# Optimization experiments

Hardware: AMD Instinct MI355X
Metric: run time of the kernel (lower is better)

Reference implementation:

```python
import jax, jax.numpy as jnp
import numpy as np

NUM_LEVELS = 6
LEVEL_DIM = 4
LOG2_HASHMAP = 19
HASHMAP_SIZE = 1 << LOG2_HASHMAP
BASE_RES = 16
DESIRED_RES = 512
SPHERE_RADIUS = 500.0
N_RAYS = 1048576
PER_LEVEL_SCALE = float(np.exp(np.log(DESIRED_RES / BASE_RES) / (NUM_LEVELS - 1)))  # = 2.0
PRIMES = (1, 2654435761, 805459861)
# static 8 trilinear corner offsets [8,3]
_CORNERS_NP = np.array([[i, j, k] for i in (0, 1) for j in (0, 1) for k in (0, 1)], dtype=np.int64)


def _level_params(level):
    # torch-ngp / Instant-NGP convention: scale = base * gamma**L - 1, res = ceil(scale)+1
    scale = BASE_RES * (PER_LEVEL_SCALE ** level) - 1.0
    res = int(np.ceil(scale)) + 1
    return scale, res


def hash_grid_encode(coords, table):
    """coords: [N,3] in [0,1]; table: [L, HASHMAP_SIZE, D] -> [N, L*D]."""
    corners_f = jnp.asarray(_CORNERS_NP, dtype=coords.dtype)        # [8,3]
    corners_u = jnp.asarray(_CORNERS_NP, dtype=jnp.uint32)          # [8,3]
    outs = []
    for level in range(NUM_LEVELS):
        scale, res = _level_params(level)
        pos = coords * scale + 0.5                                   # [N,3]
        pos_grid = jnp.floor(pos)
        frac = pos - pos_grid                                        # [N,3] in [0,1)
        pg = pos_grid.astype(jnp.uint32)                             # [N,3]
        cg = pg[:, None, :] + corners_u[None, :, :]                  # [N,8,3]
        if res ** 3 <= HASHMAP_SIZE:
            # dense indexing for coarse levels
            cg = jnp.minimum(cg, jnp.uint32(res - 1))
            idx = cg[..., 0] + cg[..., 1] * jnp.uint32(res) + cg[..., 2] * jnp.uint32(res * res)
        else:
            # spatial hash with xor of primes, table size is a power of two
            h = (cg[..., 0] * jnp.uint32(PRIMES[0])
                 ^ cg[..., 1] * jnp.uint32(PRIMES[1])
                 ^ cg[..., 2] * jnp.uint32(PRIMES[2]))
            idx = h & jnp.uint32(HASHMAP_SIZE - 1)
        feats = table[level][idx.astype(jnp.int32)]                  # [N,8,D] gather
        # trilinear weights: prod over dims of (frac if corner==1 else 1-frac)
        w = jnp.prod(jnp.where(corners_f[None] == 1.0, frac[:, None, :], 1.0 - frac[:, None, :]), axis=-1)  # [N,8]
        outs.append(jnp.sum(feats * w[..., None], axis=1))           # [N,D]
    return jnp.concatenate(outs, axis=-1)                            # [N, L*D]


def setup_inputs() -> dict:
    key = jax.random.key(0)
    k1, k2, k3 = jax.random.split(key, 3)
    view_dirs = jax.random.normal(k1, (N_RAYS, 3), dtype=jnp.float32)
    view_dirs = view_dirs / jnp.linalg.norm(view_dirs, axis=-1, keepdims=True)
    ray_origins = jax.random.normal(k2, (N_RAYS, 3), dtype=jnp.float32)  # cameras near origin, radius >> extent
    table = jax.random.uniform(k3, (NUM_LEVELS, HASHMAP_SIZE, LEVEL_DIM),
                               dtype=jnp.float32, minval=-0.1, maxval=0.1)
    return {"view_dirs": view_dirs, "ray_origins": ray_origins, "table": table}


def reference(view_dirs, ray_origins, table):
    # ray-sphere intersection (a=1 since dirs normalized)
    b = 2.0 * jnp.sum(ray_origins * view_dirs, axis=-1, keepdims=True)
    c = jnp.sum(ray_origins * ray_origins, axis=-1, keepdims=True) - SPHERE_RADIUS ** 2
    disc = b * b - 4.0 * c
    t = (-b + jnp.sqrt(jnp.maximum(disc, 0.0))) / 2.0
    pts = ray_origins + t * view_dirs                                 # [N,3]
    coords = jnp.clip((pts + SPHERE_RADIUS) / (2.0 * SPHERE_RADIUS), 0.0, 1.0)
    return hash_grid_encode(coords, table)                            # [N, 24]
```

## Files before the change

kernel.cpp:

```cpp
#include <hip/hip_runtime.h>

constexpr unsigned kHashmapSize = 1u << 19;
constexpr float kSphereR = 500.0f;

__global__ __launch_bounds__(256)
void sphere_hashgrid_kernel(const float* __restrict__ dirs,
                            const float* __restrict__ orig,
                            const float4* __restrict__ table4,
                            float* __restrict__ out,
                            int n_rays)
{
    int n = blockIdx.x * blockDim.x + threadIdx.x;
    if (n >= n_rays) return;

    float dx = dirs[3 * n + 0], dy = dirs[3 * n + 1], dz = dirs[3 * n + 2];
    float ox = orig[3 * n + 0], oy = orig[3 * n + 1], oz = orig[3 * n + 2];

    float b = 2.0f * ((ox * dx + oy * dy) + oz * dz);
    float c = ((ox * ox + oy * oy) + oz * oz) - kSphereR * kSphereR;
    float disc = b * b - 4.0f * c;
    float t = (-b + sqrtf(fmaxf(disc, 0.0f))) * 0.5f;
    float px = ox + t * dx, py = oy + t * dy, pz = oz + t * dz;

    float cx = fminf(fmaxf((px + kSphereR) / (2.0f * kSphereR), 0.0f), 1.0f);
    float cy = fminf(fmaxf((py + kSphereR) / (2.0f * kSphereR), 0.0f), 1.0f);
    float cz = fminf(fmaxf((pz + kSphereR) / (2.0f * kSphereR), 0.0f), 1.0f);

    constexpr float kScale[6] = {15.f, 31.f, 63.f, 127.f, 255.f, 511.f};
    constexpr unsigned kRes[6] = {16u, 32u, 64u, 128u, 256u, 512u};

    float* outp = out + (size_t)n * 24;

#pragma unroll
    for (int L = 0; L < 6; ++L) {
        const float sc = kScale[L];
        const unsigned res = kRes[L];
        const bool dense = (L < 3);

        float posx = cx * sc + 0.5f;
        float posy = cy * sc + 0.5f;
        float posz = cz * sc + 0.5f;
        float gx_f = floorf(posx), gy_f = floorf(posy), gz_f = floorf(posz);
        float fx = posx - gx_f, fy = posy - gy_f, fz = posz - gz_f;
        unsigned gx = (unsigned)gx_f, gy = (unsigned)gy_f, gz = (unsigned)gz_f;

        const float4* __restrict__ tl = table4 + (size_t)L * kHashmapSize;

        unsigned idx[8];
#pragma unroll
        for (int cr = 0; cr < 8; ++cr) {
            unsigned i = (unsigned)(cr >> 2);
            unsigned j = (unsigned)((cr >> 1) & 1);
            unsigned k = (unsigned)(cr & 1);
            unsigned x = gx + i, y = gy + j, z = gz + k;
            if (dense) {
                x = min(x, res - 1u);
                y = min(y, res - 1u);
                z = min(z, res - 1u);
                idx[cr] = x + y * res + z * res * res;
            } else {
                idx[cr] = (x * 1u ^ y * 2654435761u ^ z * 805459861u) & (kHashmapSize - 1u);
            }
        }

        float4 f[8];
#pragma unroll
        for (int cr = 0; cr < 8; ++cr) f[cr] = tl[idx[cr]];

        float wx[2] = {1.0f - fx, fx};
        float wy[2] = {1.0f - fy, fy};
        float wz[2] = {1.0f - fz, fz};

        float4 acc = make_float4(0.f, 0.f, 0.f, 0.f);
#pragma unroll
        for (int cr = 0; cr < 8; ++cr) {
            float w = (wx[(cr >> 2) & 1] * wy[(cr >> 1) & 1]) * wz[cr & 1];
            acc.x += f[cr].x * w;
            acc.y += f[cr].y * w;
            acc.z += f[cr].z * w;
            acc.w += f[cr].w * w;
        }

        *(float4*)(outp + L * 4) = acc;
    }
}

extern "C" void kernel_launch(void* const* d_in, const int* in_sizes, int n_in,
                              void* d_out, int out_size, void* d_ws, size_t ws_size,
                              hipStream_t stream) {
    const float* dirs = (const float*)d_in[0];
    const float* orig = (const float*)d_in[1];
    const float4* table4 = (const float4*)d_in[2];
    float* out = (float*)d_out;

    int n_rays = in_sizes[0] / 3;
    const int block = 256;
    int grid = (n_rays + block - 1) / block;
    sphere_hashgrid_kernel<<<grid, block, 0, stream>>>(dirs, orig, table4, out, n_rays);
}
```

Measured before the change: 446.0 us.

## Sort rays by Morton-coded spatial bucket before hash-grid encoding

Adds a counting sort of rays into 32^3 Morton-ordered spatial buckets: a histogram pass, a single-block scan, and an atomic scatter that writes the normalized coordinates plus the ray id into a workspace. The encode kernel then reads the sorted rays, so neighbouring threads gather nearby table entries, and it uses a block-index swizzle. The goal is better cache locality for the random table gathers. The cost is four extra launches, recomputing the ray intersection twice, contended atomics, a serial scan, and scattered 96-byte output writes.

New measurement: 410.5 us. 8.0% less time.

```diff
diff --git a/kernel.cpp b/kernel.cpp
--- a/kernel.cpp
+++ b/kernel.cpp
@@ -2,34 +2,112 @@
 
 constexpr unsigned kHashmapSize = 1u << 19;
 constexpr float kSphereR = 500.0f;
+constexpr int kLog2Buckets = 15;
+constexpr int kNumBuckets = 1 << kLog2Buckets;
 
-__global__ __launch_bounds__(256)
-void sphere_hashgrid_kernel(const float* __restrict__ dirs,
-                            const float* __restrict__ orig,
-                            const float4* __restrict__ table4,
-                            float* __restrict__ out,
-                            int n_rays)
-{
-    int n = blockIdx.x * blockDim.x + threadIdx.x;
-    if (n >= n_rays) return;
+typedef float v4f __attribute__((ext_vector_type(4)));
 
+__device__ __forceinline__ unsigned part1by2(unsigned x) {
+    x &= 0x3FFu;
+    x = (x | (x << 16)) & 0x030000FFu;
+    x = (x | (x << 8))  & 0x0300F00Fu;
+    x = (x | (x << 4))  & 0x030C30C3u;
+    x = (x | (x << 2))  & 0x09249249u;
+    return x;
+}
+
+__device__ __forceinline__ void ray_coords(const float* __restrict__ dirs,
+                                           const float* __restrict__ orig,
+                                           int n, float& cx, float& cy, float& cz) {
     float dx = dirs[3 * n + 0], dy = dirs[3 * n + 1], dz = dirs[3 * n + 2];
     float ox = orig[3 * n + 0], oy = orig[3 * n + 1], oz = orig[3 * n + 2];
-
     float b = 2.0f * ((ox * dx + oy * dy) + oz * dz);
     float c = ((ox * ox + oy * oy) + oz * oz) - kSphereR * kSphereR;
     float disc = b * b - 4.0f * c;
     float t = (-b + sqrtf(fmaxf(disc, 0.0f))) * 0.5f;
     float px = ox + t * dx, py = oy + t * dy, pz = oz + t * dz;
+    cx = fminf(fmaxf((px + kSphereR) / (2.0f * kSphereR), 0.0f), 1.0f);
+    cy = fminf(fmaxf((py + kSphereR) / (2.0f * kSphereR), 0.0f), 1.0f);
+    cz = fminf(fmaxf((pz + kSphereR) / (2.0f * kSphereR), 0.0f), 1.0f);
+}
 
-    float cx = fminf(fmaxf((px + kSphereR) / (2.0f * kSphereR), 0.0f), 1.0f);
-    float cy = fminf(fmaxf((py + kSphereR) / (2.0f * kSphereR), 0.0f), 1.0f);
-    float cz = fminf(fmaxf((pz + kSphereR) / (2.0f * kSphereR), 0.0f), 1.0f);
+__device__ __forceinline__ unsigned bucket_of(float cx, float cy, float cz) {
+    unsigned qx = min(31u, (unsigned)(cx * 32.0f));
+    unsigned qy = min(31u, (unsigned)(cy * 32.0f));
+    unsigned qz = min(31u, (unsigned)(cz * 32.0f));
+    return part1by2(qx) | (part1by2(qy) << 1) | (part1by2(qz) << 2);
+}
+
+__global__ __launch_bounds__(256)
+void zero_hist_kernel(unsigned* __restrict__ hist) {
+    int i = blockIdx.x * 256 + threadIdx.x;
+    if (i < kNumBuckets) hist[i] = 0u;
+}
+
+__global__ __launch_bounds__(256)
+void hist_kernel(const float* __restrict__ dirs, const float* __restrict__ orig,
+                 unsigned* __restrict__ hist, int n_rays) {
+    int n = blockIdx.x * 256 + threadIdx.x;
+    if (n >= n_rays) return;
+    float cx, cy, cz;
+    ray_coords(dirs, orig, n, cx, cy, cz);
+    atomicAdd(&hist[bucket_of(cx, cy, cz)], 1u);
+}
+
+__global__ __launch_bounds__(1024)
+void scan_kernel(unsigned* __restrict__ hist) {
+    __shared__ unsigned sums[1024];
+    const int t = threadIdx.x;
+    constexpr int kPer = kNumBuckets / 1024;
+    unsigned local[kPer];
+    unsigned s = 0;
+#pragma unroll
+    for (int i = 0; i < kPer; ++i) { local[i] = hist[t * kPer + i]; s += local[i]; }
+    sums[t] = s;
+    __syncthreads();
+    for (int off = 1; off < 1024; off <<= 1) {
+        unsigned v = (t >= off) ? sums[t - off] : 0u;
+        __syncthreads();
+        sums[t] += v;
+        __syncthreads();
+    }
+    unsigned run = (t == 0) ? 0u : sums[t - 1];
+#pragma unroll
+    for (int i = 0; i < kPer; ++i) { unsigned c = local[i]; hist[t * kPer + i] = run; run += c; }
+}
+
+__global__ __launch_bounds__(256)
+void scatter_kernel(const float* __restrict__ dirs, const float* __restrict__ orig,
+                    unsigned* __restrict__ offs, v4f* __restrict__ sorted, int n_rays) {
+    int n = blockIdx.x * 256 + threadIdx.x;
+    if (n >= n_rays) return;
+    float cx, cy, cz;
+    ray_coords(dirs, orig, n, cx, cy, cz);
+    unsigned key = bucket_of(cx, cy, cz);
+    unsigned pos = atomicAdd(&offs[key], 1u);
+    v4f v; v.x = cx; v.y = cy; v.z = cz; v.w = __uint_as_float((unsigned)n);
+    sorted[pos] = v;
+}
+
+__global__ __launch_bounds__(256)
+void encode_kernel(const v4f* __restrict__ sorted,
+                   const float4* __restrict__ table4,
+                   float* __restrict__ out,
+                   int n_rays, int nblocks) {
+    int bid = blockIdx.x;
+    int chunk = nblocks >> 3;
+    int swz = (bid & 7) * chunk + (bid >> 3);
+    int i = swz * 256 + (int)threadIdx.x;
+    if (i >= n_rays) return;
+
+    v4f s = sorted[i];
+    float cx = s.x, cy = s.y, cz = s.z;
+    unsigned rayid = __float_as_uint(s.w);
 
     constexpr float kScale[6] = {15.f, 31.f, 63.f, 127.f, 255.f, 511.f};
     constexpr unsigned kRes[6] = {16u, 32u, 64u, 128u, 256u, 512u};
 
-    float* outp = out + (size_t)n * 24;
+    float* outp = out + (size_t)rayid * 24;
 
 #pragma unroll
     for (int L = 0; L < 6; ++L) {
@@ -49,10 +127,10 @@
         unsigned idx[8];
 #pragma unroll
         for (int cr = 0; cr < 8; ++cr) {
-            unsigned i = (unsigned)(cr >> 2);
-            unsigned j = (unsigned)((cr >> 1) & 1);
-            unsigned k = (unsigned)(cr & 1);
-            unsigned x = gx + i, y = gy + j, z = gz + k;
+            unsigned ii = (unsigned)(cr >> 2);
+            unsigned jj = (unsigned)((cr >> 1) & 1);
+            unsigned kk = (unsigned)(cr & 1);
+            unsigned x = gx + ii, y = gy + jj, z = gz + kk;
             if (dense) {
                 x = min(x, res - 1u);
                 y = min(y, res - 1u);
@@ -94,7 +172,16 @@
     float* out = (float*)d_out;
 
     int n_rays = in_sizes[0] / 3;
+
+    v4f* sorted = (v4f*)d_ws;
+    unsigned* hist = (unsigned*)((char*)d_ws + (size_t)n_rays * 16);
+
     const int block = 256;
     int grid = (n_rays + block - 1) / block;
-    sphere_hashgrid_kernel<<<grid, block, 0, stream>>>(dirs, orig, table4, out, n_rays);
+
+    zero_hist_kernel<<<(kNumBuckets + 255) / 256, block, 0, stream>>>(hist);
+    hist_kernel<<<grid, block, 0, stream>>>(dirs, orig, hist, n_rays);
+    scan_kernel<<<1, 1024, 0, stream>>>(hist);
+    scatter_kernel<<<grid, block, 0, stream>>>(dirs, orig, hist, sorted, n_rays);
+    encode_kernel<<<grid, block, 0, stream>>>(sorted, table4, out, n_rays, grid);
 }
```
